# Kernel tuning notes

Hardware: AMD Instinct MI355X
Metric: run time of the kernel (lower is better)

The kernel has to match this reference:

```python
import jax, jax.numpy as jnp
import numpy as np


def rotary_pos_emb(x):
    # x: [..., seq, dim], dim even. Interleaved (GPT-NeoX-style pairwise) rotary.
    dim, seq = x.shape[-1], x.shape[-2]
    ts = jnp.arange(0, dim, 2, dtype=jnp.float32)
    inv_freqs = 10000.0 ** (-ts / dim)
    grid = jnp.arange(seq, dtype=jnp.float32)[:, None] * inv_freqs[None, :]  # [s, dim//2]
    sin = jnp.repeat(jnp.sin(grid), 2, axis=-1).astype(x.dtype)  # [s, dim]
    cos = jnp.repeat(jnp.cos(grid), 2, axis=-1).astype(x.dtype)  # [s, dim]
    x1, x2 = x[..., ::2], x[..., 1::2]
    xs = jnp.stack([-x2, x1], axis=-1).reshape(x.shape)  # interleave (-x2, x1)
    return x * cos + xs * sin


def setup_inputs() -> dict:
    key = jax.random.key(0)
    kx, kq, kk, kv, ko = jax.random.split(key, 5)
    B, S, D = 2, 2048, 1024
    scale = 1.0 / np.sqrt(D)
    x = jax.random.normal(kx, (B, S, D), dtype=jnp.float32)
    mask = jnp.tril(jnp.ones((S, S), dtype=bool))  # causal
    Wq = jax.random.normal(kq, (D, D), dtype=jnp.float32) * scale
    Wk = jax.random.normal(kk, (D, D), dtype=jnp.float32) * scale
    Wv = jax.random.normal(kv, (D, D), dtype=jnp.float32) * scale
    Wo = jax.random.normal(ko, (D, D), dtype=jnp.float32) * scale
    return {"x": x, "mask": mask, "Wq": Wq, "Wk": Wk, "Wv": Wv, "Wo": Wo}


def reference(x, mask, Wq, Wk, Wv, Wo):
    H = 16
    POS_PORTION = 0.5
    B, S, D = x.shape
    K = D // H
    p = int(K * POS_PORTION)

    q = (x @ Wq) / (K ** 0.5)
    q = q.reshape(B, S, H, K).transpose(0, 2, 1, 3)  # b h l k
    q = jnp.concatenate([rotary_pos_emb(q[..., :p]), q[..., p:]], axis=-1)

    k = (x @ Wk).reshape(B, S, H, K).transpose(0, 2, 1, 3)
    k = jnp.concatenate([rotary_pos_emb(k[..., :p]), k[..., p:]], axis=-1)

    v = (x @ Wv).reshape(B, S, H, K).transpose(0, 2, 1, 3)

    logits = jnp.einsum('bhik,bhjk->bhij', q, k)
    # full-precision masked softmax
    l32 = logits.astype(jnp.float32)
    l32 = jnp.where(mask, l32, -1e30)
    a = jax.nn.softmax(l32, axis=-1).astype(logits.dtype)

    y = jnp.einsum('bhij,bhjv->bhiv', a, v)
    y = y.transpose(0, 2, 1, 3).reshape(B, S, D)  # b l (h v)
    return y @ Wo
```

## Files before the change

kernel.cpp:

```cpp
#include <hip/hip_runtime.h>
#include <cstdint>
#include <cstddef>

typedef __bf16 bf16;
typedef __bf16 bf16x8 __attribute__((ext_vector_type(8)));
typedef float  f32x4  __attribute__((ext_vector_type(4)));

#define B_  2
#define S_  2048
#define D_  1024
#define H_  16
#define KH  64

__device__ __forceinline__ void gload_lds16(const bf16* gp, bf16* lds_base) {
    __builtin_amdgcn_global_load_lds(
        (const __attribute__((address_space(1))) unsigned int*)gp,
        (__attribute__((address_space(3))) unsigned int*)lds_base,
        16, 0, 0);
}

__global__ __launch_bounds__(256) void prep(
    const float* __restrict__ x, bf16* __restrict__ xb,
    const float* __restrict__ Wq, const float* __restrict__ Wk,
    const float* __restrict__ Wv, const float* __restrict__ Wo,
    bf16* __restrict__ WqkvT, bf16* __restrict__ WoT)
{
    __shared__ bf16 tl[64][72];
    int z = blockIdx.x;
    if (z < 4096) {
        const int i = (z * 256 + threadIdx.x) * 4;
        const float4 v = *(const float4*)(x + i);
        union { int2 w; bf16 e[4]; } u;
        u.e[0] = (bf16)v.x; u.e[1] = (bf16)v.y;
        u.e[2] = (bf16)v.z; u.e[3] = (bf16)v.w;
        *(int2*)(xb + i) = u.w;
        return;
    }
    z -= 4096;
    const int zx = z & 15, zy = (z >> 4) & 15, zw = z >> 8;
    const float* src = (zw == 0) ? Wq : (zw == 1) ? Wk : (zw == 2) ? Wv : Wo;
    bf16* dst = (zw < 3) ? (WqkvT + (size_t)zw * D_ * D_) : WoT;
    const int r0 = zy * 64;
    const int c0 = zx * 64;
    const int t  = threadIdx.x;
    {
        const int r = t >> 2, cs = (t & 3) * 16;
        const float4* p = (const float4*)(src + (size_t)(r0 + r) * D_ + c0 + cs);
        float4 a0 = p[0], a1 = p[1], a2 = p[2], a3 = p[3];
        tl[cs +  0][r] = (bf16)a0.x; tl[cs +  1][r] = (bf16)a0.y;
        tl[cs +  2][r] = (bf16)a0.z; tl[cs +  3][r] = (bf16)a0.w;
        tl[cs +  4][r] = (bf16)a1.x; tl[cs +  5][r] = (bf16)a1.y;
        tl[cs +  6][r] = (bf16)a1.z; tl[cs +  7][r] = (bf16)a1.w;
        tl[cs +  8][r] = (bf16)a2.x; tl[cs +  9][r] = (bf16)a2.y;
        tl[cs + 10][r] = (bf16)a2.z; tl[cs + 11][r] = (bf16)a2.w;
        tl[cs + 12][r] = (bf16)a3.x; tl[cs + 13][r] = (bf16)a3.y;
        tl[cs + 14][r] = (bf16)a3.z; tl[cs + 15][r] = (bf16)a3.w;
    }
    __syncthreads();
    {
        const int c = t >> 2, rs = (t & 3) * 16;
        union { int4 v[2]; bf16 e[16]; } u;
#pragma unroll
        for (int i = 0; i < 16; ++i) u.e[i] = tl[c][rs + i];
        int4* p = (int4*)(dst + (size_t)(c0 + c) * D_ + r0 + rs);
        p[0] = u.v[0]; p[1] = u.v[1];
    }
}

template <int EPI, int BN>
__global__ __launch_bounds__(256, 2) void gemm_bt(
    const bf16* __restrict__ A, const bf16* __restrict__ BT,
    float* __restrict__ C, int N, int Kd,
    bf16* __restrict__ qp, bf16* __restrict__ kp, bf16* __restrict__ vp)
{
    constexpr int NJF = BN / 32;
    __shared__ bf16 As[128 * 64];
    __shared__ bf16 Bs[BN * 64];
    const int tid  = threadIdx.x;
    const int lane = tid & 63;
    const int wave = tid >> 6;
    const int l15  = lane & 15;
    const int quad = lane >> 4;
    const int m0 = blockIdx.y * 128;
    const int n0 = blockIdx.x * BN;
    const int wm = (wave >> 1) * 64;
    const int wn = (wave & 1) * (BN / 2);

    f32x4 acc[4][NJF];
#pragma unroll
    for (int i = 0; i < 4; ++i)
#pragma unroll
        for (int j = 0; j < NJF; ++j) acc[i][j] = f32x4{0.f, 0.f, 0.f, 0.f};

    for (int k0 = 0; k0 < Kd; k0 += 64) {
        __syncthreads();
#pragma unroll
        for (int c = 0; c < 4; ++c) {
            const int base  = wave * 4096 + c * 1024;
            const int flatb = base + lane * 16;
            const int row   = flatb >> 7;
            const int col   = (flatb & 127) >> 1;
            gload_lds16(A + (size_t)(m0 + row) * Kd + k0 + col, As + (base >> 1));
        }
#pragma unroll
        for (int c = 0; c < NJF; ++c) {
            const int base  = wave * (BN * 32) + c * 1024;
            const int flatb = base + lane * 16;
            const int row   = flatb >> 7;
            const int col   = (flatb & 127) >> 1;
            gload_lds16(BT + (size_t)(n0 + row) * Kd + k0 + col, Bs + (base >> 1));
        }
        __syncthreads();
#pragma unroll
        for (int kk = 0; kk < 64; kk += 32) {
            bf16x8 af[4], bfv[NJF];
#pragma unroll
            for (int i = 0; i < 4; ++i)
                af[i] = *(const bf16x8*)&As[(wm + i * 16 + l15) * 64 + kk + quad * 8];
#pragma unroll
            for (int j = 0; j < NJF; ++j)
                bfv[j] = *(const bf16x8*)&Bs[(wn + j * 16 + l15) * 64 + kk + quad * 8];
#pragma unroll
            for (int i = 0; i < 4; ++i)
#pragma unroll
                for (int j = 0; j < NJF; ++j)
                    acc[i][j] = __builtin_amdgcn_mfma_f32_16x16x32_bf16(
                        af[i], bfv[j], acc[i][j], 0, 0, 0);
        }
    }

#pragma unroll
    for (int i = 0; i < 4; ++i)
#pragma unroll
        for (int j = 0; j < NJF; ++j) {
            const int Rb = m0 + wm + i * 16 + quad * 4;
            const int Cc = n0 + wn + j * 16 + l15;
            if (EPI == 0) {
#pragma unroll
                for (int r = 0; r < 4; ++r)
                    C[(size_t)(Rb + r) * N + Cc] = acc[i][j][r];
            } else {
                const int sec = Cc >> 10, cc = Cc & 1023;
                const int h = cc >> 6, kd = cc & 63;
#pragma unroll
                for (int r = 0; r < 4; ++r) {
                    const int row = Rb + r;
                    const int b = row >> 11, s = row & (S_ - 1);
                    const float v = acc[i][j][r];
                    if (sec == 0)
                        qp[((size_t)(b * H_ + h) * S_ + s) * KH + kd] =
                            (bf16)(v * 0.1803368801111204f);
                    else if (sec == 1)
                        kp[((size_t)(b * H_ + h) * S_ + s) * KH + kd] = (bf16)v;
                    else
                        vp[((size_t)(b * H_ + h) * KH + kd) * S_ + s] = (bf16)v;
                }
            }
        }
}

__global__ __launch_bounds__(256) void rope_qk(bf16* __restrict__ q, bf16* __restrict__ k)
{
    const int tid   = blockIdx.x * blockDim.x + threadIdx.x;
    const int which = tid >> 16;
    const int rem   = tid & 65535;
    const int s     = rem & (S_ - 1);
    bf16* p = (which ? k : q) + (size_t)rem * KH;
    union { int4 v[4]; bf16 e[32]; } u;
    int4* pv = (int4*)p;
#pragma unroll
    for (int i = 0; i < 4; ++i) u.v[i] = pv[i];
    const float l2_10000 = 13.28771237954945f;
#pragma unroll
    for (int i = 0; i < 16; ++i) {
        const float inv = exp2f(-(float)i * (l2_10000 / 16.f));
        const float ang = (float)s * inv;
        const float sb = sinf(ang);
        const float cb = cosf(ang);
        const float x0 = (float)u.e[2 * i], x1 = (float)u.e[2 * i + 1];
        u.e[2 * i]     = (bf16)(x0 * cb - x1 * sb);
        u.e[2 * i + 1] = (bf16)(x1 * cb + x0 * sb);
    }
#pragma unroll
    for (int i = 0; i < 4; ++i) pv[i] = u.v[i];
}

__global__ __launch_bounds__(256, 3) void attn(
    const bf16* __restrict__ q, const bf16* __restrict__ k,
    const bf16* __restrict__ vt, bf16* __restrict__ y)
{
    __shared__ bf16 Ks[2][64 * 64];
    __shared__ bf16 VTs[2][64 * 64];
    __shared__ bf16 Ps[4][16][68];

    const int z  = blockIdx.x;
    const int bh = z >> 4;
    const int pp = z & 15;
    const int b  = bh >> 4, h = bh & 15;
    const int t    = threadIdx.x;
    const int lane = t & 63, wave = t >> 6;
    const int l15  = lane & 15, quad = lane >> 4;

    const bf16* kbh = k  + (size_t)bh * S_ * KH;
    const bf16* vbh = vt + (size_t)bh * KH * S_;

    const int srow = lane >> 3;
    const int sg   = (lane & 7) ^ srow;

    auto stage = [&](int jt, int bb) {
        const int j0 = jt * 64;
#pragma unroll
        for (int i = 0; i < 2; ++i) {
            const int c = wave * 2 + i;
            gload_lds16(kbh + (size_t)(j0 + c * 8 + srow) * KH + sg * 8,
                        &Ks[bb][c * 8 * 64]);
            gload_lds16(vbh + (size_t)(c * 8 + srow) * S_ + j0 + sg * 8,
                        &VTs[bb][c * 8 * 64]);
        }
    };

#pragma unroll
    for (int phase = 0; phase < 2; ++phase) {
        const int qt   = phase ? pp : (31 - pp);
        const int wrow = qt * 64 + wave * 16;
        const int nj   = qt + 1;

        bf16x8 qf[2];
        {
            const bf16* qp = q + ((size_t)bh * S_ + wrow + l15) * KH + quad * 8;
            qf[0] = *(const bf16x8*)qp;
            qf[1] = *(const bf16x8*)(qp + 32);
        }

        f32x4 accO[4];
        float lsum[4];
#pragma unroll
        for (int j = 0; j < 4; ++j) accO[j] = f32x4{0.f, 0.f, 0.f, 0.f};
#pragma unroll
        for (int r = 0; r < 4; ++r) lsum[r] = 0.f;

        __syncthreads();
        stage(0, 0);
        for (int jt = 0; jt < nj; ++jt) {
            const int bb = jt & 1;
            __syncthreads();
            if (jt + 1 < nj) stage(jt + 1, bb ^ 1);

            f32x4 accS[4];
#pragma unroll
            for (int nb = 0; nb < 4; ++nb) accS[nb] = f32x4{0.f, 0.f, 0.f, 0.f};
#pragma unroll
            for (int c = 0; c < 2; ++c) {
                bf16x8 kf[4];
#pragma unroll
                for (int nb = 0; nb < 4; ++nb)
                    kf[nb] = *(const bf16x8*)
                        &Ks[bb][(nb * 16 + l15) * 64 + (((c * 4 + quad) ^ (l15 & 7)) * 8)];
#pragma unroll
                for (int nb = 0; nb < 4; ++nb)
                    accS[nb] = __builtin_amdgcn_mfma_f32_16x16x32_bf16(
                        qf[c], kf[nb], accS[nb], 0, 0, 0);
            }

            if (jt == nj - 1) {
                const int j0 = jt * 64;
#pragma unroll
                for (int nb = 0; nb < 4; ++nb)
#pragma unroll
                    for (int r = 0; r < 4; ++r) {
                        const int qi = wrow + quad * 4 + r;
                        const int ki = j0 + nb * 16 + l15;
                        if (ki > qi) accS[nb][r] = -1e30f;
                    }
            }

#pragma unroll
            for (int nb = 0; nb < 4; ++nb)
#pragma unroll
                for (int r = 0; r < 4; ++r) {
                    const float p = __builtin_amdgcn_exp2f(accS[nb][r]);
                    lsum[r] += p;
                    Ps[wave][quad * 4 + r][nb * 16 + l15] = (bf16)p;
                }

#pragma unroll
            for (int c = 0; c < 2; ++c) {
                bf16x8 vf[4];
#pragma unroll
                for (int vb = 0; vb < 4; ++vb)
                    vf[vb] = *(const bf16x8*)
                        &VTs[bb][(vb * 16 + l15) * 64 + (((c * 4 + quad) ^ (l15 & 7)) * 8)];
                bf16x8 pf = *(const bf16x8*)&Ps[wave][l15][c * 32 + quad * 8];
#pragma unroll
                for (int vb = 0; vb < 4; ++vb)
                    accO[vb] = __builtin_amdgcn_mfma_f32_16x16x32_bf16(
                        pf, vf[vb], accO[vb], 0, 0, 0);
            }
        }

#pragma unroll
        for (int r = 0; r < 4; ++r) {
            float s = lsum[r];
            s += __shfl_xor(s, 1);
            s += __shfl_xor(s, 2);
            s += __shfl_xor(s, 4);
            s += __shfl_xor(s, 8);
            lsum[r] = s;
        }

#pragma unroll
        for (int vb = 0; vb < 4; ++vb)
#pragma unroll
            for (int r = 0; r < 4; ++r) {
                const int row = wrow + quad * 4 + r;
                const int col = h * KH + vb * 16 + l15;
                y[((size_t)b * S_ + row) * D_ + col] = (bf16)(accO[vb][r] / lsum[r]);
            }
    }
}

extern "C" void kernel_launch(void* const* d_in, const int* in_sizes, int n_in,
                              void* d_out, int out_size, void* d_ws, size_t ws_size,
                              hipStream_t stream)
{
    (void)in_sizes; (void)n_in; (void)out_size; (void)ws_size;
    const float* x  = (const float*)d_in[0];
    const float* Wq = (const float*)d_in[2];
    const float* Wk = (const float*)d_in[3];
    const float* Wv = (const float*)d_in[4];
    const float* Wo = (const float*)d_in[5];
    float* out = (float*)d_out;

    char* ws = (char*)d_ws;
    bf16* WqkvT = (bf16*)(ws + 0);
    bf16* WoT   = (bf16*)(ws + 6291456);
    bf16* xb    = (bf16*)(ws + 8388608);
    bf16* qw    = (bf16*)(ws + 16777216);
    bf16* kw    = (bf16*)(ws + 25165824);
    bf16* vtw   = (bf16*)(ws + 33554432);
    bf16* yw    = (bf16*)(ws + 41943040);

    hipLaunchKernelGGL(prep, dim3(5120), dim3(256), 0, stream,
                       x, xb, Wq, Wk, Wv, Wo, WqkvT, WoT);
    hipLaunchKernelGGL((gemm_bt<1, 128>), dim3(24, 32), dim3(256), 0, stream,
                       xb, WqkvT, (float*)nullptr, 3072, 1024, qw, kw, vtw);
    hipLaunchKernelGGL(rope_qk, dim3(512), dim3(256), 0, stream, qw, kw);
    hipLaunchKernelGGL(attn, dim3(512), dim3(256), 0, stream, qw, kw, vtw, yw);
    hipLaunchKernelGGL((gemm_bt<0, 64>), dim3(16, 32), dim3(256), 0, stream,
                       yw, WoT, out, 1024, 1024,
                       (bf16*)nullptr, (bf16*)nullptr, (bf16*)nullptr);
}
```

Before: 211.7 us.

## Fuse Q rope into attention, split query tiles per block, MFMA row sums

After: 218.9 us. +3.4%, slower.

```diff
diff --git a/kernel.cpp b/kernel.cpp
--- a/kernel.cpp
+++ b/kernel.cpp
@@ -159,13 +159,11 @@
         }
 }
 
-__global__ __launch_bounds__(256) void rope_qk(bf16* __restrict__ q, bf16* __restrict__ k)
-{
-    const int tid   = blockIdx.x * blockDim.x + threadIdx.x;
-    const int which = tid >> 16;
-    const int rem   = tid & 65535;
-    const int s     = rem & (S_ - 1);
-    bf16* p = (which ? k : q) + (size_t)rem * KH;
+__global__ __launch_bounds__(256) void rope_k(bf16* __restrict__ k)
+{
+    const int tid = blockIdx.x * blockDim.x + threadIdx.x;
+    const int s   = tid & (S_ - 1);
+    bf16* p = k + (size_t)tid * KH;
     union { int4 v[4]; bf16 e[32]; } u;
     int4* pv = (int4*)p;
 #pragma unroll
@@ -185,21 +183,22 @@
     for (int i = 0; i < 4; ++i) pv[i] = u.v[i];
 }
 
-__global__ __launch_bounds__(256, 3) void attn(
+__global__ __launch_bounds__(256, 4) void attn(
     const bf16* __restrict__ q, const bf16* __restrict__ k,
     const bf16* __restrict__ vt, bf16* __restrict__ y)
 {
     __shared__ bf16 Ks[2][64 * 64];
     __shared__ bf16 VTs[2][64 * 64];
-    __shared__ bf16 Ps[4][16][68];
+    __shared__ bf16 Ps[4][16][64];
 
     const int z  = blockIdx.x;
-    const int bh = z >> 4;
-    const int pp = z & 15;
+    const int bh = z >> 5;
+    const int qt = z & 31;
     const int b  = bh >> 4, h = bh & 15;
     const int t    = threadIdx.x;
     const int lane = t & 63, wave = t >> 6;
     const int l15  = lane & 15, quad = lane >> 4;
+    const int wrow = qt * 64 + wave * 16;
 
     const bf16* kbh = k  + (size_t)bh * S_ * KH;
     const bf16* vbh = vt + (size_t)bh * KH * S_;
@@ -219,104 +218,106 @@
         }
     };
 
-#pragma unroll
-    for (int phase = 0; phase < 2; ++phase) {
-        const int qt   = phase ? pp : (31 - pp);
-        const int wrow = qt * 64 + wave * 16;
-        const int nj   = qt + 1;
-
-        bf16x8 qf[2];
-        {
-            const bf16* qp = q + ((size_t)bh * S_ + wrow + l15) * KH + quad * 8;
-            qf[0] = *(const bf16x8*)qp;
-            qf[1] = *(const bf16x8*)(qp + 32);
-        }
-
-        f32x4 accO[4];
-        float lsum[4];
-#pragma unroll
-        for (int j = 0; j < 4; ++j) accO[j] = f32x4{0.f, 0.f, 0.f, 0.f};
-#pragma unroll
-        for (int r = 0; r < 4; ++r) lsum[r] = 0.f;
-
+    bf16x8 qf[2];
+    {
+        const bf16* qp = q + ((size_t)bh * S_ + wrow + l15) * KH + quad * 8;
+        qf[0] = *(const bf16x8*)qp;
+        qf[1] = *(const bf16x8*)(qp + 32);
+        const float s = (float)(wrow + l15);
+#pragma unroll
+        for (int tt = 0; tt < 4; ++tt) {
+            const int i = quad * 4 + tt;
+            const float inv = exp2f(-(float)i * (13.28771237954945f / 16.f));
+            const float ang = s * inv;
+            const float sn = sinf(ang), cn = cosf(ang);
+            const float x0 = (float)qf[0][2 * tt], x1 = (float)qf[0][2 * tt + 1];
+            qf[0][2 * tt]     = (bf16)(x0 * cn - x1 * sn);
+            qf[0][2 * tt + 1] = (bf16)(x1 * cn + x0 * sn);
+        }
+    }
+
+    bf16x8 ones;
+#pragma unroll
+    for (int i = 0; i < 8; ++i) ones[i] = (bf16)1.0f;
+
+    f32x4 accO[4], lacc;
+#pragma unroll
+    for (int j = 0; j < 4; ++j) accO[j] = f32x4{0.f, 0.f, 0.f, 0.f};
+    lacc = f32x4{0.f, 0.f, 0.f, 0.f};
+
+    const int nj = qt + 1;
+    stage(0, 0);
+    for (int jt = 0; jt < nj; ++jt) {
+        const int bb = jt & 1;
         __syncthreads();
-        stage(0, 0);
-        for (int jt = 0; jt < nj; ++jt) {
-            const int bb = jt & 1;
-            __syncthreads();
-            if (jt + 1 < nj) stage(jt + 1, bb ^ 1);
-
-            f32x4 accS[4];
-#pragma unroll
-            for (int nb = 0; nb < 4; ++nb) accS[nb] = f32x4{0.f, 0.f, 0.f, 0.f};
-#pragma unroll
-            for (int c = 0; c < 2; ++c) {
-                bf16x8 kf[4];
-#pragma unroll
-                for (int nb = 0; nb < 4; ++nb)
-                    kf[nb] = *(const bf16x8*)
-                        &Ks[bb][(nb * 16 + l15) * 64 + (((c * 4 + quad) ^ (l15 & 7)) * 8)];
-#pragma unroll
-                for (int nb = 0; nb < 4; ++nb)
-                    accS[nb] = __builtin_amdgcn_mfma_f32_16x16x32_bf16(
-                        qf[c], kf[nb], accS[nb], 0, 0, 0);
+        if (jt + 1 < nj) stage(jt + 1, bb ^ 1);
+
+        f32x4 accS[4];
+#pragma unroll
+        for (int nb = 0; nb < 4; ++nb) accS[nb] = f32x4{0.f, 0.f, 0.f, 0.f};
+#pragma unroll
+        for (int c = 0; c < 2; ++c) {
+            bf16x8 kf[4];
+#pragma unroll
+            for (int nb = 0; nb < 4; ++nb)
+                kf[nb] = *(const bf16x8*)
+                    &Ks[bb][(nb * 16 + l15) * 64 + (((c * 4 + quad) ^ (l15 & 7)) * 8)];
+#pragma unroll
+            for (int nb = 0; nb < 4; ++nb)
+                accS[nb] = __builtin_amdgcn_mfma_f32_16x16x32_bf16(
+                    qf[c], kf[nb], accS[nb], 0, 0, 0);
+        }
+
+        if (jt == nj - 1) {
+            const int j0 = jt * 64;
+#pragma unroll
+            for (int nb = 0; nb < 4; ++nb)
+#pragma unroll
+                for (int r = 0; r < 4; ++r) {
+                    const int qi = wrow + quad * 4 + r;
+                    const int ki = j0 + nb * 16 + l15;
+                    if (ki > qi) accS[nb][r] = -1e30f;
+                }
+        }
+
+#pragma unroll
+        for (int nb = 0; nb < 4; ++nb)
+#pragma unroll
+            for (int r = 0; r < 4; ++r) {
+                const float p = __builtin_amdgcn_exp2f(accS[nb][r]);
+                const int row = quad * 4 + r;
+                Ps[wave][row][(((nb * 2 + (l15 >> 3)) ^ (row & 7)) * 8) + (l15 & 7)]
+                    = (bf16)p;
             }
 
-            if (jt == nj - 1) {
-                const int j0 = jt * 64;
-#pragma unroll
-                for (int nb = 0; nb < 4; ++nb)
-#pragma unroll
-                    for (int r = 0; r < 4; ++r) {
-                        const int qi = wrow + quad * 4 + r;
-                        const int ki = j0 + nb * 16 + l15;
-                        if (ki > qi) accS[nb][r] = -1e30f;
-                    }
-            }
-
-#pragma unroll
-            for (int nb = 0; nb < 4; ++nb)
-#pragma unroll
-                for (int r = 0; r < 4; ++r) {
-                    const float p = __builtin_amdgcn_exp2f(accS[nb][r]);
-                    lsum[r] += p;
-                    Ps[wave][quad * 4 + r][nb * 16 + l15] = (bf16)p;
-                }
-
-#pragma unroll
-            for (int c = 0; c < 2; ++c) {
-                bf16x8 vf[4];
-#pragma unroll
-                for (int vb = 0; vb < 4; ++vb)
-                    vf[vb] = *(const bf16x8*)
-                        &VTs[bb][(vb * 16 + l15) * 64 + (((c * 4 + quad) ^ (l15 & 7)) * 8)];
-                bf16x8 pf = *(const bf16x8*)&Ps[wave][l15][c * 32 + quad * 8];
-#pragma unroll
-                for (int vb = 0; vb < 4; ++vb)
-                    accO[vb] = __builtin_amdgcn_mfma_f32_16x16x32_bf16(
-                        pf, vf[vb], accO[vb], 0, 0, 0);
-            }
-        }
-
+#pragma unroll
+        for (int c = 0; c < 2; ++c) {
+            bf16x8 vf[4];
+#pragma unroll
+            for (int vb = 0; vb < 4; ++vb)
+                vf[vb] = *(const bf16x8*)
+                    &VTs[bb][(vb * 16 + l15) * 64 + (((c * 4 + quad) ^ (l15 & 7)) * 8)];
+            const bf16x8 pf = *(const bf16x8*)
+                &Ps[wave][l15][((c * 4 + quad) ^ (l15 & 7)) * 8];
+#pragma unroll
+            for (int vb = 0; vb < 4; ++vb)
+                accO[vb] = __builtin_amdgcn_mfma_f32_16x16x32_bf16(
+                    pf, vf[vb], accO[vb], 0, 0, 0);
+            lacc = __builtin_amdgcn_mfma_f32_16x16x32_bf16(pf, ones, lacc, 0, 0, 0);
+        }
+    }
+
+    float rinv[4];
+#pragma unroll
+    for (int r = 0; r < 4; ++r) rinv[r] = 1.0f / lacc[r];
+#pragma unroll
+    for (int vb = 0; vb < 4; ++vb)
 #pragma unroll
         for (int r = 0; r < 4; ++r) {
-            float s = lsum[r];
-            s += __shfl_xor(s, 1);
-            s += __shfl_xor(s, 2);
-            s += __shfl_xor(s, 4);
-            s += __shfl_xor(s, 8);
-            lsum[r] = s;
-        }
-
-#pragma unroll
-        for (int vb = 0; vb < 4; ++vb)
-#pragma unroll
-            for (int r = 0; r < 4; ++r) {
-                const int row = wrow + quad * 4 + r;
-                const int col = h * KH + vb * 16 + l15;
-                y[((size_t)b * S_ + row) * D_ + col] = (bf16)(accO[vb][r] / lsum[r]);
-            }
-    }
+            const int row = wrow + quad * 4 + r;
+            const int col = h * KH + vb * 16 + l15;
+            y[((size_t)b * S_ + row) * D_ + col] = (bf16)(accO[vb][r] * rinv[r]);
+        }
 }
 
 extern "C" void kernel_launch(void* const* d_in, const int* in_sizes, int n_in,
@@ -344,8 +345,8 @@
                        x, xb, Wq, Wk, Wv, Wo, WqkvT, WoT);
     hipLaunchKernelGGL((gemm_bt<1, 128>), dim3(24, 32), dim3(256), 0, stream,
                        xb, WqkvT, (float*)nullptr, 3072, 1024, qw, kw, vtw);
-    hipLaunchKernelGGL(rope_qk, dim3(512), dim3(256), 0, stream, qw, kw);
-    hipLaunchKernelGGL(attn, dim3(512), dim3(256), 0, stream, qw, kw, vtw, yw);
+    hipLaunchKernelGGL(rope_k, dim3(256), dim3(256), 0, stream, kw);
+    hipLaunchKernelGGL(attn, dim3(1024), dim3(256), 0, stream, qw, kw, vtw, yw);
     hipLaunchKernelGGL((gemm_bt<0, 64>), dim3(16, 32), dim3(256), 0, stream,
                        yw, WoT, out, 1024, 1024,
                        (bf16*)nullptr, (bf16*)nullptr, (bf16*)nullptr);
```
